# Kernel tuning notes

Measured on AMD Instinct MI355X. Metric: run time of the kernel, lower is better.

The kernel has to match this reference:

```python
import jax, jax.numpy as jnp
import numpy as np

B, C, H, W = 16, 64, 256, 256
M1, M2 = 32, 32
SCALE = 1.0 / (C * C)


def setup_inputs() -> dict:
    key = jax.random.key(0)
    ks = jax.random.split(key, 5)
    x = jax.random.normal(ks[0], (B, C, H, W), dtype=jnp.float32)
    w1_real = SCALE * jax.random.uniform(ks[1], (C, C, M1, M2), dtype=jnp.float32)
    w1_imag = SCALE * jax.random.uniform(ks[2], (C, C, M1, M2), dtype=jnp.float32)
    w2_real = SCALE * jax.random.uniform(ks[3], (C, C, M1, M2), dtype=jnp.float32)
    w2_imag = SCALE * jax.random.uniform(ks[4], (C, C, M1, M2), dtype=jnp.float32)
    return {"x": x, "w1_real": w1_real, "w1_imag": w1_imag,
            "w2_real": w2_real, "w2_imag": w2_imag}


def reference(x, w1_real, w1_imag, w2_real, w2_imag):
    # x: (B, C, H, W) real. rfft2 over last two dims -> (B, C, H, W//2+1) complex64
    x_ft = jnp.fft.rfft2(x)
    # compl_mul2d in the source reduces to an elementwise multiply by the
    # weights summed over their FIRST (in_channels) axis:
    #   out[b,c,m1,m2] = x_ft[b,c,m1,m2] * sum_j weights[j,c,m1,m2]
    w1 = (w1_real + 1j * w1_imag).sum(axis=0)  # (C, M1, M2) complex
    w2 = (w2_real + 1j * w2_imag).sum(axis=0)  # (C, M1, M2) complex
    out_ft = jnp.zeros_like(x_ft)
    out_ft = out_ft.at[:, :, :M1, :M2].set(x_ft[:, :, :M1, :M2] * w1[None])
    out_ft = out_ft.at[:, :, -M1:, :M2].set(x_ft[:, :, -M1:, :M2] * w2[None])
    return jnp.fft.irfft2(out_ft, s=(H, W))
```

## Files before the change

kernel.cpp:

```cpp
#include <hip/hip_runtime.h>
#include <math.h>

#define TWO_PI 6.28318530717958647692f

typedef __attribute__((ext_vector_type(8))) short bf16x8;
typedef __attribute__((ext_vector_type(4))) float f32x4;
typedef __attribute__((ext_vector_type(4))) short short4v;

#define MFMA16(A,B,C) __builtin_amdgcn_mfma_f32_16x16x32_bf16((A),(B),(C),0,0,0)


#define C_B2H 0
#define C_B2L 16384
#define C_C1H 32768
#define C_C1L 49152
#define C_S1H 65536
#define C_S1L 81920
#define C_SNH 98304
#define C_SNL 114688
#define C_A1H 131072
#define C_A1L 163840
#define C_DH  196608
#define C_DL  212992

__device__ __forceinline__ unsigned short bhi(float v) {
    union { float f; unsigned u; } x; x.f = v;
    return (unsigned short)(x.u >> 16);
}
__device__ __forceinline__ float bval(unsigned short h) {
    union { unsigned u; float f; } x; x.u = ((unsigned)h) << 16;
    return x.f;
}
__device__ __forceinline__ void split2(float v, unsigned short& hi, unsigned short& lo) {
    hi = bhi(v);
    lo = bhi(v - bval(hi));
}

__global__ __launch_bounds__(256)
void const_kernel(unsigned short* __restrict__ cst) {
    int e = blockIdx.x * 256 + threadIdx.x;
    const float w0 = TWO_PI / 256.0f;
    float v; int i, baseH, baseL;
    if (e < 16384) {
        i = e; baseH = C_B2H; baseL = C_B2L;
        int j = i & 7, lane = (i >> 3) & 63, tt = i >> 9;
        int nt = tt & 3, kt = tt >> 2;
        int k = kt * 32 + (lane >> 4) * 8 + j;
        int n = nt * 16 + (lane & 15);
        int fr = n & 31;
        float s_, c_;
        sincosf(w0 * (float)((fr * k) & 255), &s_, &c_);
        v = (n < 32) ? c_ : -s_;
    } else if (e < 65536) {
        int mid = (e - 16384) >> 14;
        i = (e - 16384) & 16383;
        baseH = C_C1H + mid * 32768; baseL = baseH + 16384;
        int j = i & 7, lane = (i >> 3) & 63, tt = i >> 9;
        int mt = tt & 3, kt = tt >> 2;
        int s = mt * 16 + (lane & 15);
        int h = kt * 32 + (lane >> 4) * 8 + j;
        int f = (s < 32) ? s : s + 192;
        float s_, c_;
        sincosf(w0 * (float)((f * h) & 255), &s_, &c_);
        v = (mid == 0) ? c_ : ((mid == 1) ? s_ : -s_);
    } else if (e < 98304) {
        i = e - 65536; baseH = C_A1H; baseL = C_A1L;
        int j = i & 7, lane = (i >> 3) & 63, tt = i >> 9;
        int mt = tt & 15, kt = tt >> 4;
        int h = mt * 16 + (lane & 15);
        int k = kt * 32 + (lane >> 4) * 8 + j;
        int s = k & 63;
        int f = (s < 32) ? s : s + 192;
        float s_, c_;
        sincosf(w0 * (float)((f * h) & 255), &s_, &c_);
        v = (k < 64) ? c_ : s_;
    } else {
        i = e - 98304; baseH = C_DH; baseL = C_DL;
        int j = i & 7, lane = (i >> 3) & 63, tt = i >> 9;
        int nt = tt & 15, kt = tt >> 4;
        int wc = nt * 16 + (lane & 15);
        int k = kt * 32 + (lane >> 4) * 8 + j;
        int k2 = k & 31;
        float a = (k2 == 0) ? 1.f : 2.f;
        float s_, c_;
        sincosf(w0 * (float)((k2 * wc) & 255), &s_, &c_);
        v = (k < 32) ? a * c_ : -a * s_;
    }
    unsigned short hi, lo; split2(v, hi, lo);
    cst[baseH + i] = hi;
    cst[baseL + i] = lo;
}

__global__ __launch_bounds__(256)
void wsum_kernel(const float* __restrict__ w1r, const float* __restrict__ w1i,
                 const float* __restrict__ w2r, const float* __restrict__ w2i,
                 float2* __restrict__ s1, float2* __restrict__ s2) {
    int e = blockIdx.x * 256 + threadIdx.x;
    float a = 0.f, b = 0.f, c = 0.f, d = 0.f;
    #pragma unroll 4
    for (int j = 0; j < 64; ++j) {
        int idx = j * 65536 + e;
        a += w1r[idx]; b += w1i[idx];
        c += w2r[idx]; d += w2i[idx];
    }
    const float sc = 1.0f / 65536.0f;
    s1[e] = make_float2(a * sc, b * sc);
    s2[e] = make_float2(c * sc, d * sc);
}

__global__ __launch_bounds__(256)
void fwd_kernel(const float* __restrict__ x, float* __restrict__ X,
                const unsigned short* __restrict__ cst) {
    const int img = blockIdx.x;
    const int t = threadIdx.x;
    const int lane = t & 63;
    const int wv = t >> 6;

    __shared__ unsigned short xs_hi[8192], xs_lo[8192];
    __shared__ unsigned short yt_hi[2048], yt_lo[2048];

    f32x4 acc[4];
    #pragma unroll
    for (int i = 0; i < 4; ++i) { acc[i].x = 0; acc[i].y = 0; acc[i].z = 0; acc[i].w = 0; }

    const int mt2  = wv >> 1;
    const int nt2b = (wv & 1) * 2;

    const float* xim = x + (size_t)img * 65536;
    const int r_st  = t >> 3;
    const int c4_st = t & 7;

    #pragma unroll 1
    for (int hc = 0; hc < 8; ++hc) {
        {
            const float4* src = (const float4*)(xim + (size_t)(hc * 32 + r_st) * 256) + c4_st;
            #pragma unroll
            for (int i = 0; i < 8; ++i) {
                float4 vx = src[i * 8];
                int cc = (c4_st + i * 8) * 4;
                int idx = (r_st * 256 + cc) ^ ((r_st & 7) << 3);
                unsigned short h0,l0,h1,l1,h2,l2,h3,l3;
                split2(vx.x, h0, l0); split2(vx.y, h1, l1);
                split2(vx.z, h2, l2); split2(vx.w, h3, l3);
                short4v vh, vl;
                vh.x=(short)h0; vh.y=(short)h1; vh.z=(short)h2; vh.w=(short)h3;
                vl.x=(short)l0; vl.y=(short)l1; vl.z=(short)l2; vl.w=(short)l3;
                *(short4v*)&xs_hi[idx] = vh;
                *(short4v*)&xs_lo[idx] = vl;
            }
        }
        __syncthreads();
        f32x4 acc2[2];
        acc2[0].x=0; acc2[0].y=0; acc2[0].z=0; acc2[0].w=0;
        acc2[1].x=0; acc2[1].y=0; acc2[1].z=0; acc2[1].w=0;
        {
            const int mrow = mt2 * 16 + (lane & 15);
            const int kb = (lane >> 4) * 8;
            #pragma unroll
            for (int kt = 0; kt < 8; ++kt) {
                int aidx = (mrow * 256 + kt * 32 + kb) ^ ((mrow & 7) << 3);
                bf16x8 ah = *(const bf16x8*)&xs_hi[aidx];
                bf16x8 al = *(const bf16x8*)&xs_lo[aidx];
                #pragma unroll
                for (int q = 0; q < 2; ++q) {
                    int boff = ((kt * 4 + nt2b + q) * 64 + lane) * 8;
                    bf16x8 bh = *(const bf16x8*)&cst[C_B2H + boff];
                    bf16x8 bl = *(const bf16x8*)&cst[C_B2L + boff];
                    acc2[q] = MFMA16(ah, bh, acc2[q]);
                    acc2[q] = MFMA16(ah, bl, acc2[q]);
                    acc2[q] = MFMA16(al, bh, acc2[q]);
                }
            }
        }
        {
            const int hbase = mt2 * 16 + (lane >> 4) * 4;
            #pragma unroll
            for (int q = 0; q < 2; ++q) {
                int n = (nt2b + q) * 16 + (lane & 15);
                int idx = (n * 32 + hbase) ^ ((n & 7) << 3);
                short4v vh, vl; unsigned short hh, ll;
                split2(acc2[q][0], hh, ll); vh.x=(short)hh; vl.x=(short)ll;
                split2(acc2[q][1], hh, ll); vh.y=(short)hh; vl.y=(short)ll;
                split2(acc2[q][2], hh, ll); vh.z=(short)hh; vl.z=(short)ll;
                split2(acc2[q][3], hh, ll); vh.w=(short)hh; vl.w=(short)ll;
                *(short4v*)&yt_hi[idx] = vh;
                *(short4v*)&yt_lo[idx] = vl;
            }
        }
        __syncthreads();
        {
            const int aoff = ((hc * 4 + wv) * 64 + lane) * 8;
            bf16x8 c1h = *(const bf16x8*)&cst[C_C1H + aoff];
            bf16x8 c1l = *(const bf16x8*)&cst[C_C1L + aoff];
            bf16x8 s1h = *(const bf16x8*)&cst[C_S1H + aoff];
            bf16x8 s1l = *(const bf16x8*)&cst[C_S1L + aoff];
            bf16x8 snh = *(const bf16x8*)&cst[C_SNH + aoff];
            bf16x8 snl = *(const bf16x8*)&cst[C_SNL + aoff];
            const int kl = (lane >> 4) * 8;
            #pragma unroll
            for (int nt = 0; nt < 4; ++nt) {
                int nRe = (nt & 1) * 16 + (lane & 15);
                int nIm = 32 + nRe;
                int reIdx = (nRe * 32 + kl) ^ ((nRe & 7) << 3);
                int imIdx = (nIm * 32 + kl) ^ ((nIm & 7) << 3);
                bf16x8 brh = *(const bf16x8*)&yt_hi[reIdx];
                bf16x8 brl = *(const bf16x8*)&yt_lo[reIdx];
                bf16x8 bih = *(const bf16x8*)&yt_hi[imIdx];
                bf16x8 bil = *(const bf16x8*)&yt_lo[imIdx];
                if (nt < 2) {
                    acc[nt] = MFMA16(c1h, brh, acc[nt]);
                    acc[nt] = MFMA16(c1h, brl, acc[nt]);
                    acc[nt] = MFMA16(c1l, brh, acc[nt]);
                    acc[nt] = MFMA16(s1h, bih, acc[nt]);
                    acc[nt] = MFMA16(s1h, bil, acc[nt]);
                    acc[nt] = MFMA16(s1l, bih, acc[nt]);
                } else {
                    acc[nt] = MFMA16(c1h, bih, acc[nt]);
                    acc[nt] = MFMA16(c1h, bil, acc[nt]);
                    acc[nt] = MFMA16(c1l, bih, acc[nt]);
                    acc[nt] = MFMA16(snh, brh, acc[nt]);
                    acc[nt] = MFMA16(snh, brl, acc[nt]);
                    acc[nt] = MFMA16(snl, brh, acc[nt]);
                }
            }
        }
        __syncthreads();
    }
    {
        float* Xp = X + (size_t)img * 4096;
        const int sbase = wv * 16 + (lane >> 4) * 4;
        #pragma unroll
        for (int nt = 0; nt < 4; ++nt) {
            int n = nt * 16 + (lane & 15);
            #pragma unroll
            for (int r = 0; r < 4; ++r)
                Xp[(sbase + r) * 64 + n] = acc[nt][r];
        }
    }
}

__global__ __launch_bounds__(256)
void inv_kernel(const float* __restrict__ X, const float2* __restrict__ s1,
                const float2* __restrict__ s2, float* __restrict__ out,
                const unsigned short* __restrict__ cst) {
    const int img = blockIdx.x;
    const int c = img & 63;
    const int t = threadIdx.x;
    const int lane = t & 63;
    const int wv = t >> 6;

    __shared__ unsigned short lds[32768];
    unsigned short* GTh = lds;
    unsigned short* GTl = lds + 8192;
    unsigned short* Th  = lds;
    unsigned short* Tl  = lds + 16384;

    {
        const float* Xp = X + (size_t)img * 4096;
        int s = t >> 2;
        int k2b = (t & 3) * 8;
        const float2* wp = (s < 32) ? (s1 + c * 1024 + s * 32 + k2b)
                                    : (s2 + c * 1024 + (s - 32) * 32 + k2b);
        float4 xr0 = *(const float4*)&Xp[s * 64 + k2b];
        float4 xr1 = *(const float4*)&Xp[s * 64 + k2b + 4];
        float4 xi0 = *(const float4*)&Xp[s * 64 + 32 + k2b];
        float4 xi1 = *(const float4*)&Xp[s * 64 + 32 + k2b + 4];
        float xr[8] = {xr0.x,xr0.y,xr0.z,xr0.w,xr1.x,xr1.y,xr1.z,xr1.w};
        float xi[8] = {xi0.x,xi0.y,xi0.z,xi0.w,xi1.x,xi1.y,xi1.z,xi1.w};
        #pragma unroll
        for (int i = 0; i < 8; ++i) {
            int k2 = k2b + i;
            float2 wvv = wp[i];
            float gr = xr[i]*wvv.x - xi[i]*wvv.y;
            float gi = xr[i]*wvv.y + xi[i]*wvv.x;
            unsigned short grh, grl, gih, gil;
            split2(gr, grh, grl); split2(gi, gih, gil);
            int swz = (k2 & 7) << 3;
            int i0 = (k2 * 128 + s) ^ swz;
            int i1 = ((32 + k2) * 128 + s) ^ swz;
            int i2 = (k2 * 128 + 64 + s) ^ swz;
            int i3 = ((32 + k2) * 128 + 64 + s) ^ swz;
            GTh[i0] = grh; GTl[i0] = grl;
            GTh[i1] = gih; GTl[i1] = gil;
            GTh[i2] = (unsigned short)(gih ^ 0x8000u);
            GTl[i2] = (unsigned short)(gil ^ 0x8000u);
            GTh[i3] = grh; GTl[i3] = grl;
        }
    }
    __syncthreads();

    f32x4 Tacc[4][4];
    #pragma unroll
    for (int a = 0; a < 4; ++a)
        #pragma unroll
        for (int b = 0; b < 4; ++b) { Tacc[a][b].x=0; Tacc[a][b].y=0; Tacc[a][b].z=0; Tacc[a][b].w=0; }
    {
        const int kb = (lane >> 4) * 8;
        #pragma unroll
        for (int kt = 0; kt < 4; ++kt) {
            bf16x8 bh[4], bl[4];
            #pragma unroll
            for (int nt = 0; nt < 4; ++nt) {
                int n = nt * 16 + (lane & 15);
                int idx = (n * 128 + kt * 32 + kb) ^ ((n & 7) << 3);
                bh[nt] = *(const bf16x8*)&GTh[idx];
                bl[nt] = *(const bf16x8*)&GTl[idx];
            }
            #pragma unroll
            for (int mi = 0; mi < 4; ++mi) {
                int aoff = ((kt * 16 + 4 * wv + mi) * 64 + lane) * 8;
                bf16x8 ah = *(const bf16x8*)&cst[C_A1H + aoff];
                bf16x8 al = *(const bf16x8*)&cst[C_A1L + aoff];
                #pragma unroll
                for (int nt = 0; nt < 4; ++nt) {
                    Tacc[mi][nt] = MFMA16(ah, bh[nt], Tacc[mi][nt]);
                    Tacc[mi][nt] = MFMA16(ah, bl[nt], Tacc[mi][nt]);
                    Tacc[mi][nt] = MFMA16(al, bh[nt], Tacc[mi][nt]);
                }
            }
        }
    }
    __syncthreads();

    {
        #pragma unroll
        for (int mi = 0; mi < 4; ++mi) {
            int m0 = (4 * wv + mi) * 16 + (lane >> 4) * 4;
            #pragma unroll
            for (int nt = 0; nt < 4; ++nt) {
                int k = nt * 16 + (lane & 15);
                #pragma unroll
                for (int r = 0; r < 4; ++r) {
                    int m = m0 + r;
                    int idx = (m * 64 + k) ^ ((m & 7) << 3);
                    unsigned short hh, ll; split2(Tacc[mi][nt][r], hh, ll);
                    Th[idx] = hh; Tl[idx] = ll;
                }
            }
        }
    }
    __syncthreads();

    float* oim = out + (size_t)img * 65536;
    const int kb2 = (lane >> 4) * 8;
    #pragma unroll 1
    for (int strip = 0; strip < 4; ++strip) {
        f32x4 oacc[4][4];
        #pragma unroll
        for (int a = 0; a < 4; ++a)
            #pragma unroll
            for (int b = 0; b < 4; ++b) { oacc[a][b].x=0; oacc[a][b].y=0; oacc[a][b].z=0; oacc[a][b].w=0; }
        #pragma unroll
        for (int kt = 0; kt < 2; ++kt) {
            bf16x8 ah[4], al[4];
            #pragma unroll
            for (int mi = 0; mi < 4; ++mi) {
                int m = (strip * 4 + mi) * 16 + (lane & 15);
                int idx = (m * 64 + kt * 32 + kb2) ^ ((m & 7) << 3);
                ah[mi] = *(const bf16x8*)&Th[idx];
                al[mi] = *(const bf16x8*)&Tl[idx];
            }
            #pragma unroll
            for (int ni = 0; ni < 4; ++ni) {
                int boff = ((kt * 16 + 4 * wv + ni) * 64 + lane) * 8;
                bf16x8 bh = *(const bf16x8*)&cst[C_DH + boff];
                bf16x8 bl = *(const bf16x8*)&cst[C_DL + boff];
                #pragma unroll
                for (int mi = 0; mi < 4; ++mi) {
                    oacc[mi][ni] = MFMA16(ah[mi], bh, oacc[mi][ni]);
                    oacc[mi][ni] = MFMA16(ah[mi], bl, oacc[mi][ni]);
                    oacc[mi][ni] = MFMA16(al[mi], bh, oacc[mi][ni]);
                }
            }
        }
        #pragma unroll
        for (int mi = 0; mi < 4; ++mi) {
            int h = strip * 64 + mi * 16 + (lane >> 4) * 4;
            #pragma unroll
            for (int ni = 0; ni < 4; ++ni) {
                int wc = (4 * wv + ni) * 16 + (lane & 15);
                #pragma unroll
                for (int r = 0; r < 4; ++r)
                    oim[(size_t)(h + r) * 256 + wc] = oacc[mi][ni][r];
            }
        }
    }
}

extern "C" void kernel_launch(void* const* d_in, const int* in_sizes, int n_in,
                              void* d_out, int out_size, void* d_ws, size_t ws_size,
                              hipStream_t stream) {
    const float* x   = (const float*)d_in[0];
    const float* w1r = (const float*)d_in[1];
    const float* w1i = (const float*)d_in[2];
    const float* w2r = (const float*)d_in[3];
    const float* w2i = (const float*)d_in[4];
    float* out = (float*)d_out;

    char* ws = (char*)d_ws;
    float* X   = (float*)ws;
    float2* s1 = (float2*)(ws + 16777216);
    float2* s2 = (float2*)(ws + 16777216 + 524288);
    unsigned short* cst = (unsigned short*)(ws + 17825792);

    hipLaunchKernelGGL(const_kernel, dim3(448), dim3(256), 0, stream, cst);
    hipLaunchKernelGGL(wsum_kernel, dim3(256), dim3(256), 0, stream,
                       w1r, w1i, w2r, w2i, s1, s2);
    hipLaunchKernelGGL(fwd_kernel, dim3(1024), dim3(256), 0, stream, x, X, cst);
    hipLaunchKernelGGL(inv_kernel, dim3(1024), dim3(256), 0, stream, X, s1, s2, out, cst);
}
```

Before: 554.5 us.

## Split weight sum into vectorized two-pass reduction and prefetch input rows in fwd

Result: no change. 552.5 us (-0.4%).

```diff
diff --git a/kernel.cpp b/kernel.cpp
--- a/kernel.cpp
+++ b/kernel.cpp
@@ -92,20 +92,49 @@
 }
 
 __global__ __launch_bounds__(256)
-void wsum_kernel(const float* __restrict__ w1r, const float* __restrict__ w1i,
-                 const float* __restrict__ w2r, const float* __restrict__ w2i,
-                 float2* __restrict__ s1, float2* __restrict__ s2) {
-    int e = blockIdx.x * 256 + threadIdx.x;
-    float a = 0.f, b = 0.f, c = 0.f, d = 0.f;
-    #pragma unroll 4
-    for (int j = 0; j < 64; ++j) {
-        int idx = j * 65536 + e;
-        a += w1r[idx]; b += w1i[idx];
-        c += w2r[idx]; d += w2i[idx];
+void wsum_part(const float* __restrict__ w1r, const float* __restrict__ w1i,
+               const float* __restrict__ w2r, const float* __restrict__ w2i,
+               float4* __restrict__ part) {
+    const int jp = blockIdx.x >> 6;
+    const int e4 = (blockIdx.x & 63) * 256 + threadIdx.x;
+    const float4* A = (const float4*)w1r;
+    const float4* Bv = (const float4*)w1i;
+    const float4* Cv = (const float4*)w2r;
+    const float4* Dv = (const float4*)w2i;
+    float4 a = make_float4(0.f,0.f,0.f,0.f), b = a, c = a, d = a;
+    #pragma unroll
+    for (int jj = 0; jj < 8; ++jj) {
+        int idx = (jp * 8 + jj) * 16384 + e4;
+        float4 v;
+        v = A[idx];  a.x += v.x; a.y += v.y; a.z += v.z; a.w += v.w;
+        v = Bv[idx]; b.x += v.x; b.y += v.y; b.z += v.z; b.w += v.w;
+        v = Cv[idx]; c.x += v.x; c.y += v.y; c.z += v.z; c.w += v.w;
+        v = Dv[idx]; d.x += v.x; d.y += v.y; d.z += v.z; d.w += v.w;
+    }
+    part[(0 * 8 + jp) * 16384 + e4] = a;
+    part[(1 * 8 + jp) * 16384 + e4] = b;
+    part[(2 * 8 + jp) * 16384 + e4] = c;
+    part[(3 * 8 + jp) * 16384 + e4] = d;
+}
+
+__global__ __launch_bounds__(256)
+void wsum_reduce(const float4* __restrict__ part,
+                 float4* __restrict__ s1, float4* __restrict__ s2) {
+    const int e4 = blockIdx.x * 256 + threadIdx.x;
+    float4 a = make_float4(0.f,0.f,0.f,0.f), b = a, c = a, d = a;
+    #pragma unroll
+    for (int jp = 0; jp < 8; ++jp) {
+        float4 v;
+        v = part[(0 * 8 + jp) * 16384 + e4]; a.x += v.x; a.y += v.y; a.z += v.z; a.w += v.w;
+        v = part[(1 * 8 + jp) * 16384 + e4]; b.x += v.x; b.y += v.y; b.z += v.z; b.w += v.w;
+        v = part[(2 * 8 + jp) * 16384 + e4]; c.x += v.x; c.y += v.y; c.z += v.z; c.w += v.w;
+        v = part[(3 * 8 + jp) * 16384 + e4]; d.x += v.x; d.y += v.y; d.z += v.z; d.w += v.w;
     }
     const float sc = 1.0f / 65536.0f;
-    s1[e] = make_float2(a * sc, b * sc);
-    s2[e] = make_float2(c * sc, d * sc);
+    s1[e4 * 2]     = make_float4(a.x * sc, b.x * sc, a.y * sc, b.y * sc);
+    s1[e4 * 2 + 1] = make_float4(a.z * sc, b.z * sc, a.w * sc, b.w * sc);
+    s2[e4 * 2]     = make_float4(c.x * sc, d.x * sc, c.y * sc, d.y * sc);
+    s2[e4 * 2 + 1] = make_float4(c.z * sc, d.z * sc, c.w * sc, d.w * sc);
 }
 
 __global__ __launch_bounds__(256)
@@ -129,14 +158,18 @@
     const float* xim = x + (size_t)img * 65536;
     const int r_st  = t >> 3;
     const int c4_st = t & 7;
+    const float4* src = (const float4*)xim + r_st * 64 + c4_st;
+
+    float4 pre[8];
+    #pragma unroll
+    for (int i = 0; i < 8; ++i) pre[i] = src[i * 8];
 
     #pragma unroll 1
     for (int hc = 0; hc < 8; ++hc) {
         {
-            const float4* src = (const float4*)(xim + (size_t)(hc * 32 + r_st) * 256) + c4_st;
             #pragma unroll
             for (int i = 0; i < 8; ++i) {
-                float4 vx = src[i * 8];
+                float4 vx = pre[i];
                 int cc = (c4_st + i * 8) * 4;
                 int idx = (r_st * 256 + cc) ^ ((r_st & 7) << 3);
                 unsigned short h0,l0,h1,l1,h2,l2,h3,l3;
@@ -150,6 +183,11 @@
             }
         }
         __syncthreads();
+        if (hc < 7) {
+            const float4* nsrc = src + (hc + 1) * 2048;
+            #pragma unroll
+            for (int i = 0; i < 8; ++i) pre[i] = nsrc[i * 8];
+        }
         f32x4 acc2[2];
         acc2[0].x=0; acc2[0].y=0; acc2[0].z=0; acc2[0].w=0;
         acc2[1].x=0; acc2[1].y=0; acc2[1].z=0; acc2[1].w=0;
@@ -402,10 +440,13 @@
     float2* s1 = (float2*)(ws + 16777216);
     float2* s2 = (float2*)(ws + 16777216 + 524288);
     unsigned short* cst = (unsigned short*)(ws + 17825792);
+    float4* part = (float4*)ws;
 
     hipLaunchKernelGGL(const_kernel, dim3(448), dim3(256), 0, stream, cst);
-    hipLaunchKernelGGL(wsum_kernel, dim3(256), dim3(256), 0, stream,
-                       w1r, w1i, w2r, w2i, s1, s2);
+    hipLaunchKernelGGL(wsum_part, dim3(512), dim3(256), 0, stream,
+                       w1r, w1i, w2r, w2i, part);
+    hipLaunchKernelGGL(wsum_reduce, dim3(64), dim3(256), 0, stream,
+                       part, (float4*)s1, (float4*)s2);
     hipLaunchKernelGGL(fwd_kernel, dim3(1024), dim3(256), 0, stream, x, X, cst);
     hipLaunchKernelGGL(inv_kernel, dim3(1024), dim3(256), 0, stream, X, s1, s2, out, cst);
 }
```
